# Kernel optimization log

Hardware: AMD Instinct MI355X
Metric: run time of the kernel (lower is better)

Reference implementation:

```python
import jax, jax.numpy as jnp
import numpy as np

N = 50000      # nodes
E = 400000     # edges
DIM = 3        # pseudo-coordinate dim
M = 3          # kernel size per dim (closed B-spline, degree 1)
K = M ** DIM   # 27 basis weights
IN = 32
MID = 32
OUT = 32
EPS = 1e-5


def spline_basis(edge_attr):
    """Degree-1 closed B-spline basis. edge_attr: [E, DIM] in [0,1].
    Returns basis [E, 2^DIM], weight indices [E, 2^DIM] into K."""
    bits = (jnp.arange(2 ** DIM)[:, None] >> jnp.arange(DIM)[None, :]) & 1  # [8, DIM]
    scaled = edge_attr * M                       # closed spline: scale by kernel size
    lo = jnp.floor(scaled)
    frac = scaled - lo                           # [E, DIM]
    b = jnp.where(bits[None].astype(bool), frac[:, None, :], 1.0 - frac[:, None, :])
    basis = jnp.prod(b, axis=-1)                 # [E, 8]
    idx = (lo.astype(jnp.int32)[:, None, :] + bits[None]) % M  # [E, 8, DIM]
    strides = M ** jnp.arange(DIM)               # [1, 3, 9]
    widx = jnp.sum(idx * strides, axis=-1)       # [E, 8] in [0, K)
    return basis, widx


def spline_conv(x, src, dst, basis, widx, W, root, bias):
    """x: [N, in]; W: [K, in, out]; mean aggregation + root weight + bias."""
    x_j = x[src]                                          # gather [E, in]
    upd = basis[:, :, None] * x_j[:, None, :]             # [E, 8, in]
    # scatter-add basis-weighted source features into per-(node, weight-idx) bins
    S = jnp.zeros((N, K, x.shape[1]), x.dtype).at[dst[:, None], widx].add(upd)
    deg = jnp.zeros((N,), x.dtype).at[dst].add(1.0)
    deg = jnp.maximum(deg, 1.0)
    msg = jnp.einsum('nki,kio->no', S, W) / deg[:, None]  # mean over incoming edges
    return msg + x @ root + bias


def batchnorm(h, gamma, beta):
    mu = jnp.mean(h, axis=0)
    var = jnp.var(h, axis=0)  # biased, as in torch BN forward
    return (h - mu) * jax.lax.rsqrt(var + EPS) * gamma + beta


def setup_inputs() -> dict:
    key = jax.random.key(0)
    ks = jax.random.split(key, 16)
    d = {}
    d['x'] = jax.random.normal(ks[0], (N, IN), jnp.float32)
    d['edge_index'] = jax.random.randint(ks[1], (2, E), 0, N, dtype=jnp.int32)
    d['edge_attr'] = jax.random.uniform(ks[2], (E, DIM), dtype=jnp.float32)
    d['pos'] = jax.random.normal(ks[3], (N, DIM), jnp.float32)
    def wscale(fan_in):
        return 1.0 / np.sqrt(fan_in)
    d['W1'] = jax.random.normal(ks[4], (K, IN, MID), jnp.float32) * wscale(IN)
    d['root1'] = jax.random.normal(ks[5], (IN, MID), jnp.float32) * wscale(IN)
    d['b1'] = jnp.zeros((MID,), jnp.float32)
    d['W2'] = jax.random.normal(ks[6], (K, MID, 2 * MID), jnp.float32) * wscale(MID)
    d['root2'] = jax.random.normal(ks[7], (MID, 2 * MID), jnp.float32) * wscale(MID)
    d['b2'] = jnp.zeros((2 * MID,), jnp.float32)
    d['gamma'] = jnp.ones((2 * MID,), jnp.float32)
    d['beta'] = jnp.zeros((2 * MID,), jnp.float32)
    c3_in = 2 * MID + 3
    d['W3'] = jax.random.normal(ks[8], (K, c3_in, OUT), jnp.float32) * wscale(c3_in)
    d['root3'] = jax.random.normal(ks[9], (c3_in, OUT), jnp.float32) * wscale(c3_in)
    d['b3'] = jnp.zeros((OUT,), jnp.float32)
    return d


def reference(x, edge_index, edge_attr, pos, W1, root1, b1, W2, root2, b2,
              gamma, beta, W3, root3, b3):
    src, dst = edge_index[0], edge_index[1]
    basis, widx = spline_basis(edge_attr)
    h = jax.nn.elu(spline_conv(x, src, dst, basis, widx, W1, root1, b1))
    h = jax.nn.elu(batchnorm(spline_conv(h, src, dst, basis, widx, W2, root2, b2), gamma, beta))
    h = jnp.concatenate([h, pos], axis=1)
    out = spline_conv(h, src, dst, basis, widx, W3, root3, b3)
    return out
```

## Files before the change

kernel.cpp:

```cpp
#include <hip/hip_runtime.h>
#include <hip/hip_bf16.h>


#define EPS 1e-5f
#define MAXN 50176
#define MAXE 401408
#define SP2 904
#define SP3 2696

typedef __attribute__((ext_vector_type(8))) short short8;
typedef __attribute__((ext_vector_type(4))) float floatx4;

__device__ int             g_deg[MAXN];
__device__ int             g_offs[MAXN + 1];
__device__ int             g_cursor[MAXN];
__device__ int             g_bsum[256];
__device__ int             g_esrc[MAXE];
__device__ __align__(16) uint4 g_ebas[MAXE * 4];
__device__ __align__(16) __hip_bfloat16 g_h0[MAXN * 32];
__device__ __align__(16) __hip_bfloat16 g_h1[MAXN * 32];
__device__ __align__(16) __hip_bfloat16 g_h2[MAXN * 64];
__device__ __align__(16) __hip_bfloat16 g_h3[MAXN * 96];
__device__ __align__(16) __hip_bfloat16 g_Wp1[28672];
__device__ __align__(16) __hip_bfloat16 g_Wp2[57344];
__device__ __align__(16) __hip_bfloat16 g_Wp3[86016];
__device__ float           g_stats[128];
__device__ int             g_isbf16;

__device__ __forceinline__ float loadf(const void* p, int i, bool bf)
{
    return bf ? (float)((const __hip_bfloat16*)p)[i] : ((const float*)p)[i];
}
__device__ __forceinline__ float bf16f(unsigned int u)
{
    return __uint_as_float(u << 16);
}
__device__ __forceinline__ unsigned short bfbits(float f)
{
    union { __hip_bfloat16 h; unsigned short u; } cv;
    cv.h = __float2bfloat16(f);
    return cv.u;
}

__global__ void init_detect(const unsigned int* __restrict__ x, int n)
{
    int i = blockIdx.x * blockDim.x + threadIdx.x;
    if (blockIdx.x == 0 && threadIdx.x < 64) {
        int lane = threadIdx.x;
        int cnt = 0;
        for (int k = lane; k < 256; k += 64) {
            unsigned int lo = x[k] & 0xFFFFu;
            int ex = (int)((lo >> 7) & 0xFFu);
            if (lo == 0u || (ex >= 96 && ex <= 140)) cnt++;
        }
#pragma unroll
        for (int o = 1; o < 64; o <<= 1) cnt += __shfl_xor(cnt, o, 64);
        if (lane == 0) g_isbf16 = (cnt >= 200) ? 1 : 0;
    }
    if (i < n) { g_deg[i] = 0; g_cursor[i] = 0; }
    if (i < 128) g_stats[i] = 0.0f;
}

template <int COUT>
__device__ __forceinline__ void prep_ws_dev(const void* W, const void* root,
                                            __hip_bfloat16* Wp, int t, bool bf)
{
    int j = t & 7;
    int lane = (t >> 3) & 63;
    int rest = t >> 9;
    int kk = rest % 28;
    int nt = rest / 28;
    int k = kk * 32 + (lane >> 4) * 8 + j;
    int o = nt * 16 + (lane & 15);
    float v = (k < 864) ? loadf(W, k * COUT + o, bf)
                        : loadf(root, (k - 864) * COUT + o, bf);
    Wp[t] = __float2bfloat16(v);
}

__device__ __forceinline__ void prep_w3_dev(const void* W, const void* root,
                                            __hip_bfloat16* Wp, int t, bool bf)
{
    const int KB = 84;
    int j = t & 7;
    int lane = (t >> 3) & 63;
    int rest = t >> 9;
    int kk = rest % KB;
    int nt = rest / KB;
    int k = kk * 32 + (lane >> 4) * 8 + j;
    int o = nt * 16 + (lane & 15);
    float v = 0.0f;
    if (k < 2592) {
        int bin = k / 96;
        int ch = k - bin * 96;
        if (ch < 67) v = loadf(W, (bin * 67 + ch) * 32 + o, bf);
    } else {
        int ch = k - 2592;
        if (ch < 67) v = loadf(root, ch * 32 + o, bf);
    }
    Wp[t] = __float2bfloat16(v);
}

__global__ void misc_kernel(const int* __restrict__ dst, const void* __restrict__ x,
                            const void* W1, const void* r1,
                            const void* W2, const void* r2,
                            const void* W3, const void* r3, int E, int N)
{
    int t = blockIdx.x * blockDim.x + threadIdx.x;
    const bool bf = (g_isbf16 != 0);
    if (t < E) { atomicAdd(&g_deg[dst[t]], 1); return; }
    t -= E;
    int nx = N * 32;
    if (t < nx) { g_h0[t] = __float2bfloat16(loadf(x, t, bf)); return; }
    t -= nx;
    if (t < 28672) { prep_ws_dev<32>(W1, r1, g_Wp1, t, bf); return; }
    t -= 28672;
    if (t < 57344) { prep_ws_dev<64>(W2, r2, g_Wp2, t, bf); return; }
    t -= 57344;
    if (t < 86016) { prep_w3_dev(W3, r3, g_Wp3, t, bf); return; }
}

__global__ void scan_blk(int n)
{
    __shared__ int buf[256];
    int tid = threadIdx.x;
    int i = blockIdx.x * 256 + tid;
    int v = (i < n) ? g_deg[i] : 0;
    buf[tid] = v;
    __syncthreads();
    for (int o = 1; o < 256; o <<= 1) {
        int t = (tid >= o) ? buf[tid - o] : 0;
        __syncthreads();
        buf[tid] += t;
        __syncthreads();
    }
    if (i < n) g_offs[i] = buf[tid] - v;
    if (tid == 255) g_bsum[blockIdx.x] = buf[255];
}

__global__ void scan_top(int nb, int n)
{
    __shared__ int buf[256];
    int tid = threadIdx.x;
    int v = (tid < nb) ? g_bsum[tid] : 0;
    buf[tid] = v;
    __syncthreads();
    for (int o = 1; o < 256; o <<= 1) {
        int t = (tid >= o) ? buf[tid - o] : 0;
        __syncthreads();
        buf[tid] += t;
        __syncthreads();
    }
    if (tid < nb) g_bsum[tid] = buf[tid] - v;
    if (tid == nb - 1) g_offs[n] = buf[tid];
}

__global__ void scan_add(int n)
{
    int i = blockIdx.x * 256 + threadIdx.x;
    if (i < n) g_offs[i] += g_bsum[i >> 8];
}

__global__ void basis_fill(const void* __restrict__ attr,
                           const int* __restrict__ src,
                           const int* __restrict__ dst, int E)
{
    int e = blockIdx.x * blockDim.x + threadIdx.x;
    if (e >= E) return;
    const bool bf = (g_isbf16 != 0);
    float f[3];
    int lo[3];
#pragma unroll
    for (int d = 0; d < 3; ++d) {
        float a = loadf(attr, e * 3 + d, bf);
        float s = a * 3.0f;
        float l = floorf(s);
        lo[d] = (int)l;
        f[d] = s - l;
    }
    const int p3[3] = {1, 3, 9};
    int wx8[8];
    unsigned short bb[8];
#pragma unroll
    for (int b = 0; b < 8; ++b) {
        float w = 1.0f;
        int id = 0;
#pragma unroll
        for (int d = 0; d < 3; ++d) {
            int bit = (b >> d) & 1;
            w *= bit ? f[d] : (1.0f - f[d]);
            id += ((lo[d] + bit) % 3) * p3[d];
        }
        wx8[b] = id;
        bb[b] = bfbits(w);
    }
    unsigned wds[16];
#pragma unroll
    for (int i = 0; i < 16; ++i) {
        unsigned w = 0;
#pragma unroll
        for (int b = 0; b < 8; ++b) {
            if (wx8[b] == 2 * i)     w |= (unsigned)bb[b];
            if (wx8[b] == 2 * i + 1) w |= (unsigned)bb[b] << 16;
        }
        wds[i] = w;
    }
    int d = dst[e];
    int p = atomicAdd(&g_cursor[d], 1);
    int slot = g_offs[d] + p;
    uint4* out4 = &g_ebas[(size_t)slot * 4];
    out4[0] = make_uint4(wds[0],  wds[1],  wds[2],  wds[3]);
    out4[1] = make_uint4(wds[4],  wds[5],  wds[6],  wds[7]);
    out4[2] = make_uint4(wds[8],  wds[9],  wds[10], wds[11]);
    out4[3] = make_uint4(wds[12], wds[13], wds[14], wds[15]);
    g_esrc[slot] = src[e];
}

template <int COUT, bool ELU, int IN_SEL, int OUT_SEL>
__global__ __launch_bounds__(512, 8) void fused_conv(const void* __restrict__ bias,
                                                     int N)
{
    __shared__ unsigned short Sb[8 * SP2];
    __shared__ float invd[8];
    int tid = threadIdx.x, wid = tid >> 6, lane = tid & 63;
    int nbase = blockIdx.x * 8;
    const bool bf = (g_isbf16 != 0);
    const unsigned short* xptr = (IN_SEL == 0) ? (const unsigned short*)g_h0
                                               : (const unsigned short*)g_h1;
    const __hip_bfloat16* Wp = (COUT == 32) ? g_Wp1 : g_Wp2;

    int n = nbase + wid;
    int m = lane & 15, quad = lane >> 4;

    if (n < N) {
        int e0 = g_offs[n], e1 = g_offs[n + 1];
        floatx4 C00 = {}, C01 = {}, C10 = {}, C11 = {};
        for (int base = e0; base < e1; base += 32) {
            int cnt = e1 - base; if (cnt > 32) cnt = 32;
            int jmax = (cnt + 3) >> 2;
            unsigned a0w[4] = {0, 0, 0, 0}, a1w[4] = {0, 0, 0, 0};
            unsigned b0w[4] = {0, 0, 0, 0}, b1w[4] = {0, 0, 0, 0};
#pragma unroll
            for (int j = 0; j < 8; ++j) {
                if (j >= jmax) break;
                int kidx = j * 4 + quad;
                int e = base + kidx;
                int sn = 0;
                unsigned p0 = 0, p1 = 0;
                if (kidx < cnt) {
                    sn = g_esrc[e];
                    const unsigned short* brow =
                        (const unsigned short*)&g_ebas[(size_t)e * 4];
                    p0 = brow[m];
                    p1 = brow[16 + m];
                }
                unsigned av0 = xptr[(size_t)sn * 32 + m];
                unsigned av1 = xptr[(size_t)sn * 32 + 16 + m];
                unsigned sh = 16 * (j & 1);
                a0w[j >> 1] |= av0 << sh;
                a1w[j >> 1] |= av1 << sh;
                b0w[j >> 1] |= p0 << sh;
                b1w[j >> 1] |= p1 << sh;
            }
            union U { unsigned w[4]; short8 v; } A0, A1, B0, B1;
#pragma unroll
            for (int q = 0; q < 4; ++q) {
                A0.w[q] = a0w[q]; A1.w[q] = a1w[q];
                B0.w[q] = b0w[q]; B1.w[q] = b1w[q];
            }
            C00 = __builtin_amdgcn_mfma_f32_16x16x32_bf16(A0.v, B0.v, C00, 0, 0, 0);
            C01 = __builtin_amdgcn_mfma_f32_16x16x32_bf16(A0.v, B1.v, C01, 0, 0, 0);
            C10 = __builtin_amdgcn_mfma_f32_16x16x32_bf16(A1.v, B0.v, C10, 0, 0, 0);
            C11 = __builtin_amdgcn_mfma_f32_16x16x32_bf16(A1.v, B1.v, C11, 0, 0, 0);
        }
        unsigned short* Srow = Sb + wid * SP2;
        {
            floatx4 Cf[4] = {C00, C01, C10, C11};
#pragma unroll
            for (int f = 0; f < 4; ++f) {
                int mt = f >> 1, nt = f & 1;
                int bin = nt * 16 + m;
                if (bin < 27) {
                    union { unsigned short h[4]; uint2 u; } pk;
#pragma unroll
                    for (int r = 0; r < 4; ++r) pk.h[r] = bfbits(Cf[f][r]);
                    *(uint2*)(Srow + bin * 32 + mt * 16 + quad * 4) = pk.u;
                }
            }
        }
        if (lane < 32) Srow[864 + lane] = xptr[(size_t)n * 32 + lane];
        if (lane == 0) {
            int deg = e1 - e0;
            invd[wid] = 1.0f / (float)(deg < 1 ? 1 : deg);
        }
    }
    __syncthreads();

    if (wid * 16 < COUT) {
        int mrow = m & 7;
        const unsigned short* Ab = Sb + mrow * SP2 + quad * 8;
        floatx4 accS = {}, accR = {};
#pragma unroll
        for (int kk = 0; kk < 28; ++kk) {
            short8 a = *(const short8*)(Ab + kk * 32);
            const short* bp = (const short*)Wp +
                ((size_t)(wid * 28 + kk) * 64 + lane) * 8;
            short8 b = *(const short8*)bp;
            if (kk < 27) accS = __builtin_amdgcn_mfma_f32_16x16x32_bf16(a, b, accS, 0, 0, 0);
            else         accR = __builtin_amdgcn_mfma_f32_16x16x32_bf16(a, b, accR, 0, 0, 0);
        }
        int o = wid * 16 + m;
        float bval = loadf(bias, o, bf);
#pragma unroll
        for (int r = 0; r < 4; ++r) {
            int slot = quad * 4 + r;
            if (slot >= 8) continue;
            int nn = nbase + slot;
            if (nn >= N) continue;
            float v = accS[r] * invd[slot] + accR[r] + bval;
            if (ELU) v = v > 0.0f ? v : expm1f(v);
            if (OUT_SEL == 1) g_h1[nn * 32 + o] = __float2bfloat16(v);
            else              g_h2[nn * 64 + o] = __float2bfloat16(v);
        }
    }
}

__global__ __launch_bounds__(512, 4) void fused_conv3(const void* __restrict__ bias,
                                                      void* __restrict__ out_ext,
                                                      int N)
{
    __shared__ __align__(16) unsigned short Sb[8 * SP3];
    __shared__ float red[6][64][4];
    __shared__ float invd[8];
    int tid = threadIdx.x, wid = tid >> 6, lane = tid & 63;
    int nbase = blockIdx.x * 8;
    const bool bf = (g_isbf16 != 0);
    const unsigned short* xptr = (const unsigned short*)g_h3;

    int n = nbase + wid;
    int m = lane & 15, quad = lane >> 4;

    if (n < N) {
        int e0 = g_offs[n], e1 = g_offs[n + 1];
        floatx4 C[6][2];
#pragma unroll
        for (int t = 0; t < 6; ++t) {
            C[t][0] = (floatx4){0.f, 0.f, 0.f, 0.f};
            C[t][1] = (floatx4){0.f, 0.f, 0.f, 0.f};
        }
        for (int base = e0; base < e1; base += 32) {
            int cnt = e1 - base; if (cnt > 32) cnt = 32;
            int jmax = (cnt + 3) >> 2;
            unsigned aw[6][4] = {{0, 0, 0, 0}, {0, 0, 0, 0}, {0, 0, 0, 0},
                                 {0, 0, 0, 0}, {0, 0, 0, 0}, {0, 0, 0, 0}};
            unsigned b0w[4] = {0, 0, 0, 0}, b1w[4] = {0, 0, 0, 0};
#pragma unroll
            for (int j = 0; j < 8; ++j) {
                if (j >= jmax) break;
                int kidx = j * 4 + quad;
                int e = base + kidx;
                int sn = 0;
                unsigned p0 = 0, p1 = 0;
                if (kidx < cnt) {
                    sn = g_esrc[e];
                    const unsigned short* brow =
                        (const unsigned short*)&g_ebas[(size_t)e * 4];
                    p0 = brow[m];
                    p1 = brow[16 + m];
                }
                const unsigned short* hr = xptr + (size_t)sn * 96 + m;
                unsigned av[6];
#pragma unroll
                for (int t = 0; t < 6; ++t) av[t] = hr[t * 16];
                unsigned sh = 16 * (j & 1);
#pragma unroll
                for (int t = 0; t < 6; ++t) aw[t][j >> 1] |= av[t] << sh;
                b0w[j >> 1] |= p0 << sh;
                b1w[j >> 1] |= p1 << sh;
            }
            union U { unsigned w[4]; short8 v; } A, B0, B1;
#pragma unroll
            for (int q = 0; q < 4; ++q) { B0.w[q] = b0w[q]; B1.w[q] = b1w[q]; }
#pragma unroll
            for (int t = 0; t < 6; ++t) {
#pragma unroll
                for (int q = 0; q < 4; ++q) A.w[q] = aw[t][q];
                C[t][0] = __builtin_amdgcn_mfma_f32_16x16x32_bf16(A.v, B0.v, C[t][0], 0, 0, 0);
                C[t][1] = __builtin_amdgcn_mfma_f32_16x16x32_bf16(A.v, B1.v, C[t][1], 0, 0, 0);
            }
        }
        unsigned short* Srow = Sb + wid * SP3;
#pragma unroll
        for (int t = 0; t < 6; ++t) {
#pragma unroll
            for (int ntile = 0; ntile < 2; ++ntile) {
                int bin = ntile * 16 + m;
                if (bin < 27) {
                    union { unsigned short h[4]; uint2 uu; } pk;
#pragma unroll
                    for (int r = 0; r < 4; ++r) pk.h[r] = bfbits(C[t][ntile][r]);
                    *(uint2*)(Srow + bin * 96 + t * 16 + quad * 4) = pk.uu;
                }
            }
        }
        for (int t2 = lane; t2 < 96; t2 += 64)
            Srow[2592 + t2] = xptr[(size_t)n * 96 + t2];
        if (lane == 0) {
            int deg = e1 - e0;
            invd[wid] = 1.0f / (float)(deg < 1 ? 1 : deg);
        }
    }
    __syncthreads();

    int nt = wid & 1, kq = wid >> 1;
    int mrow = m & 7;
    const unsigned short* Ab = Sb + mrow * SP3 + quad * 8;
    floatx4 accS = {}, accR = {};
    {
        int kbeg = kq * 21, kend = kbeg + 21;
        int ksplit = (kend < 81) ? kend : 81;
        for (int kk = kbeg; kk < ksplit; ++kk) {
            short8 a = *(const short8*)(Ab + kk * 32);
            const short* bp = (const short*)g_Wp3 +
                ((size_t)(nt * 84 + kk) * 64 + lane) * 8;
            short8 b = *(const short8*)bp;
            accS = __builtin_amdgcn_mfma_f32_16x16x32_bf16(a, b, accS, 0, 0, 0);
        }
        for (int kk = ksplit; kk < kend; ++kk) {
            short8 a = *(const short8*)(Ab + kk * 32);
            const short* bp = (const short*)g_Wp3 +
                ((size_t)(nt * 84 + kk) * 64 + lane) * 8;
            short8 b = *(const short8*)bp;
            accR = __builtin_amdgcn_mfma_f32_16x16x32_bf16(a, b, accR, 0, 0, 0);
        }
    }
    if (kq < 3)
        *(floatx4*)&red[wid][lane][0] = accS;
    __syncthreads();
    if (kq == 3) {
#pragma unroll
        for (int w = 0; w < 3; ++w)
            accS += *(const floatx4*)&red[2 * w + nt][lane][0];
        int o = nt * 16 + m;
        float bval = loadf(bias, o, bf);
#pragma unroll
        for (int r = 0; r < 4; ++r) {
            int slot = quad * 4 + r;
            if (slot >= 8) continue;
            int nn = nbase + slot;
            if (nn >= N) continue;
            float v = accS[r] * invd[slot] + accR[r] + bval;
            if (bf) ((__hip_bfloat16*)out_ext)[nn * 32 + o] = __float2bfloat16(v);
            else    ((float*)out_ext)[nn * 32 + o] = v;
        }
    }
}

__global__ void bn_reduce(int n)
{
    int tid = threadIdx.x;
    int c = tid & 63;
    int r = tid >> 6;
    float s = 0.0f, s2 = 0.0f;
    for (int i = blockIdx.x * 4 + r; i < n; i += gridDim.x * 4) {
        float v = (float)g_h2[i * 64 + c];
        s += v; s2 += v * v;
    }
    __shared__ float b1s[256], b2s[256];
    b1s[tid] = s; b2s[tid] = s2;
    __syncthreads();
    if (r == 0) {
        s  = b1s[c] + b1s[c + 64] + b1s[c + 128] + b1s[c + 192];
        s2 = b2s[c] + b2s[c + 64] + b2s[c + 128] + b2s[c + 192];
        atomicAdd(&g_stats[c], s);
        atomicAdd(&g_stats[64 + c], s2);
    }
}

__global__ void h3_build(const void* __restrict__ pos,
                         const void* __restrict__ gamma,
                         const void* __restrict__ beta, int N)
{
    __shared__ float cf[128];
    int t = threadIdx.x;
    const bool bf = (g_isbf16 != 0);
    if (t < 64) {
        float inv_n = 1.0f / (float)N;
        float mu = g_stats[t] * inv_n;
        float var = g_stats[64 + t] * inv_n - mu * mu;
        float A = rsqrtf(var + EPS) * loadf(gamma, t, bf);
        cf[t] = A;
        cf[64 + t] = loadf(beta, t, bf) - mu * A;
    }
    __syncthreads();
    int idx = blockIdx.x * blockDim.x + t;
    if (idx >= N * 96) return;
    int n = idx / 96, ch = idx - n * 96;
    float v;
    if (ch < 64) {
        float h = (float)g_h2[n * 64 + ch];
        v = h * cf[ch] + cf[64 + ch];
        v = v > 0.0f ? v : expm1f(v);
    } else if (ch < 67) {
        v = loadf(pos, n * 3 + (ch - 64), bf);
    } else {
        v = 0.0f;
    }
    g_h3[(size_t)n * 96 + ch] = __float2bfloat16(v);
}

extern "C" void kernel_launch(void* const* d_in, const int* in_sizes, int n_in,
                              void* d_out, int out_size, void* d_ws, size_t ws_size,
                              hipStream_t stream)
{
    const void* x      = d_in[0];
    const int*  eindex = (const int*)d_in[1];
    const void* eattr  = d_in[2];
    const void* pos    = d_in[3];
    const void* W1     = d_in[4];
    const void* root1  = d_in[5];
    const void* b1     = d_in[6];
    const void* W2     = d_in[7];
    const void* root2  = d_in[8];
    const void* b2     = d_in[9];
    const void* gamma  = d_in[10];
    const void* beta   = d_in[11];
    const void* W3     = d_in[12];
    const void* root3  = d_in[13];
    const void* b3     = d_in[14];
    (void)d_ws; (void)ws_size; (void)n_in; (void)out_size;

    const int N = in_sizes[0] / 32;
    const int E = in_sizes[1] / 2;
    const int* srcp = eindex;
    const int* dstp = eindex + E;

    init_detect<<<(N + 255) / 256, 256, 0, stream>>>((const unsigned int*)x, N);
    {
        int tot = E + N * 32 + 28672 + 57344 + 86016;
        misc_kernel<<<(tot + 255) / 256, 256, 0, stream>>>(
            dstp, x, W1, root1, W2, root2, W3, root3, E, N);
    }
    int nb = (N + 255) / 256;
    scan_blk<<<nb, 256, 0, stream>>>(N);
    scan_top<<<1, 256, 0, stream>>>(nb, N);
    scan_add<<<nb, 256, 0, stream>>>(N);
    basis_fill<<<(E + 255) / 256, 256, 0, stream>>>(eattr, srcp, dstp, E);

    int nb8 = (N + 7) / 8;
    fused_conv<32, true, 0, 1><<<nb8, 512, 0, stream>>>(b1, N);
    fused_conv<64, false, 1, 2><<<nb8, 512, 0, stream>>>(b2, N);
    bn_reduce<<<120, 256, 0, stream>>>(N);
    h3_build<<<(N * 96 + 255) / 256, 256, 0, stream>>>(pos, gamma, beta, N);
    fused_conv3<<<nb8, 512, 0, stream>>>(b3, d_out, N);
}
```

Before: 431.7 us.

## Permute channel and basis layouts for packed dword gathers and stage edges in LDS

Reorders the basis bins and feature channels so each lane fetches adjacent bf16 pairs as a single 32-bit load. The weight-prep permutation is changed to match. Per-edge basis rows and source indices are staged cooperatively into shared memory, 16 edges per chunk, replacing scattered global 16-bit loads. The aim is fewer, wider global memory transactions in the gather phase. In exchange the MFMA K dimension is half filled per chunk (16 of 32 slots), which doubles MFMA issue count, and it relies on s_waitcnt without a barrier for intra-wave LDS visibility.

```diff
diff --git a/kernel.cpp b/kernel.cpp
--- a/kernel.cpp
+++ b/kernel.cpp
@@ -72,8 +72,16 @@
     int nt = rest / 28;
     int k = kk * 32 + (lane >> 4) * 8 + j;
     int o = nt * 16 + (lane & 15);
-    float v = (k < 864) ? loadf(W, k * COUT + o, bf)
-                        : loadf(root, (k - 864) * COUT + o, bf);
+    float v;
+    if (k < 864) {
+        int bin = k >> 5, p = k & 31;
+        int ch = 2 * (p & 15) + (p >> 4);
+        v = loadf(W, (bin * 32 + ch) * COUT + o, bf);
+    } else {
+        int p = k - 864;
+        int ch = 2 * (p & 15) + (p >> 4);
+        v = loadf(root, ch * COUT + o, bf);
+    }
     Wp[t] = __float2bfloat16(v);
 }
 
@@ -91,10 +99,12 @@
     float v = 0.0f;
     if (k < 2592) {
         int bin = k / 96;
-        int ch = k - bin * 96;
+        int p = k - bin * 96;
+        int ch = 6 * (p & 15) + (p >> 4);
         if (ch < 67) v = loadf(W, (bin * 67 + ch) * 32 + o, bf);
     } else {
-        int ch = k - 2592;
+        int p = k - 2592;
+        int ch = 6 * (p & 15) + (p >> 4);
         if (ch < 67) v = loadf(root, ch * 32 + o, bf);
     }
     Wp[t] = __float2bfloat16(v);
@@ -199,8 +209,8 @@
         unsigned w = 0;
 #pragma unroll
         for (int b = 0; b < 8; ++b) {
-            if (wx8[b] == 2 * i)     w |= (unsigned)bb[b];
-            if (wx8[b] == 2 * i + 1) w |= (unsigned)bb[b] << 16;
+            if (wx8[b] == i)      w |= (unsigned)bb[b];
+            if (wx8[b] == i + 16) w |= (unsigned)bb[b] << 16;
         }
         wds[i] = w;
     }
@@ -220,6 +230,8 @@
                                                      int N)
 {
     __shared__ unsigned short Sb[8 * SP2];
+    __shared__ __align__(16) unsigned basb[8][16][16];
+    __shared__ int ssrc[8][16];
     __shared__ float invd[8];
     int tid = threadIdx.x, wid = tid >> 6, lane = tid & 63;
     int nbase = blockIdx.x * 8;
@@ -234,32 +246,32 @@
     if (n < N) {
         int e0 = g_offs[n], e1 = g_offs[n + 1];
         floatx4 C00 = {}, C01 = {}, C10 = {}, C11 = {};
-        for (int base = e0; base < e1; base += 32) {
-            int cnt = e1 - base; if (cnt > 32) cnt = 32;
+        for (int base = e0; base < e1; base += 16) {
+            int cnt = e1 - base; if (cnt > 16) cnt = 16;
+            {
+                int es = lane >> 2, part = lane & 3;
+                uint4 v = make_uint4(0, 0, 0, 0);
+                if (es < cnt) v = g_ebas[(size_t)(base + es) * 4 + part];
+                *(uint4*)&basb[wid][es][part * 4] = v;
+                if (lane < 16)
+                    ssrc[wid][lane] = (lane < cnt) ? g_esrc[base + lane] : 0;
+            }
+            __builtin_amdgcn_s_waitcnt(0);
             int jmax = (cnt + 3) >> 2;
             unsigned a0w[4] = {0, 0, 0, 0}, a1w[4] = {0, 0, 0, 0};
             unsigned b0w[4] = {0, 0, 0, 0}, b1w[4] = {0, 0, 0, 0};
 #pragma unroll
-            for (int j = 0; j < 8; ++j) {
+            for (int j = 0; j < 4; ++j) {
                 if (j >= jmax) break;
                 int kidx = j * 4 + quad;
-                int e = base + kidx;
-                int sn = 0;
-                unsigned p0 = 0, p1 = 0;
-                if (kidx < cnt) {
-                    sn = g_esrc[e];
-                    const unsigned short* brow =
-                        (const unsigned short*)&g_ebas[(size_t)e * 4];
-                    p0 = brow[m];
-                    p1 = brow[16 + m];
-                }
-                unsigned av0 = xptr[(size_t)sn * 32 + m];
-                unsigned av1 = xptr[(size_t)sn * 32 + 16 + m];
+                int sn = ssrc[wid][kidx];
+                unsigned pw = basb[wid][kidx][m];
+                unsigned hw = *((const unsigned*)xptr + (size_t)sn * 16 + m);
                 unsigned sh = 16 * (j & 1);
-                a0w[j >> 1] |= av0 << sh;
-                a1w[j >> 1] |= av1 << sh;
-                b0w[j >> 1] |= p0 << sh;
-                b1w[j >> 1] |= p1 << sh;
+                a0w[j >> 1] |= (hw & 0xFFFFu) << sh;
+                a1w[j >> 1] |= (hw >> 16) << sh;
+                b0w[j >> 1] |= (pw & 0xFFFFu) << sh;
+                b1w[j >> 1] |= (pw >> 16) << sh;
             }
             union U { unsigned w[4]; short8 v; } A0, A1, B0, B1;
 #pragma unroll
@@ -287,7 +299,10 @@
                 }
             }
         }
-        if (lane < 32) Srow[864 + lane] = xptr[(size_t)n * 32 + lane];
+        if (lane < 32) {
+            int ch = 2 * (lane & 15) + (lane >> 4);
+            Srow[864 + lane] = xptr[(size_t)n * 32 + ch];
+        }
         if (lane == 0) {
             int deg = e1 - e0;
             invd[wid] = 1.0f / (float)(deg < 1 ? 1 : deg);
@@ -329,7 +344,10 @@
                                                       int N)
 {
     __shared__ __align__(16) unsigned short Sb[8 * SP3];
-    __shared__ float red[6][64][4];
+    __shared__ __align__(16) union {
+        struct { unsigned bas[8][16][16]; int src[8][16]; } s1;
+        float red[6][64][4];
+    } u;
     __shared__ float invd[8];
     int tid = threadIdx.x, wid = tid >> 6, lane = tid & 63;
     int nbase = blockIdx.x * 8;
@@ -347,35 +365,39 @@
             C[t][0] = (floatx4){0.f, 0.f, 0.f, 0.f};
             C[t][1] = (floatx4){0.f, 0.f, 0.f, 0.f};
         }
-        for (int base = e0; base < e1; base += 32) {
-            int cnt = e1 - base; if (cnt > 32) cnt = 32;
+        for (int base = e0; base < e1; base += 16) {
+            int cnt = e1 - base; if (cnt > 16) cnt = 16;
+            {
+                int es = lane >> 2, part = lane & 3;
+                uint4 v = make_uint4(0, 0, 0, 0);
+                if (es < cnt) v = g_ebas[(size_t)(base + es) * 4 + part];
+                *(uint4*)&u.s1.bas[wid][es][part * 4] = v;
+                if (lane < 16)
+                    u.s1.src[wid][lane] = (lane < cnt) ? g_esrc[base + lane] : 0;
+            }
+            __builtin_amdgcn_s_waitcnt(0);
             int jmax = (cnt + 3) >> 2;
             unsigned aw[6][4] = {{0, 0, 0, 0}, {0, 0, 0, 0}, {0, 0, 0, 0},
                                  {0, 0, 0, 0}, {0, 0, 0, 0}, {0, 0, 0, 0}};
             unsigned b0w[4] = {0, 0, 0, 0}, b1w[4] = {0, 0, 0, 0};
 #pragma unroll
-            for (int j = 0; j < 8; ++j) {
+            for (int j = 0; j < 4; ++j) {
                 if (j >= jmax) break;
                 int kidx = j * 4 + quad;
-                int e = base + kidx;
-                int sn = 0;
-                unsigned p0 = 0, p1 = 0;
-                if (kidx < cnt) {
-                    sn = g_esrc[e];
-                    const unsigned short* brow =
-                        (const unsigned short*)&g_ebas[(size_t)e * 4];
-                    p0 = brow[m];
-                    p1 = brow[16 + m];
-                }
-                const unsigned short* hr = xptr + (size_t)sn * 96 + m;
-                unsigned av[6];
-#pragma unroll
-                for (int t = 0; t < 6; ++t) av[t] = hr[t * 16];
+                int sn = u.s1.src[wid][kidx];
+                unsigned pw = u.s1.bas[wid][kidx][m];
+                const unsigned* hp = (const unsigned*)xptr + (size_t)sn * 48 + m * 3;
+                unsigned h0 = hp[0], h1 = hp[1], h2 = hp[2];
                 unsigned sh = 16 * (j & 1);
-#pragma unroll
-                for (int t = 0; t < 6; ++t) aw[t][j >> 1] |= av[t] << sh;
-                b0w[j >> 1] |= p0 << sh;
-                b1w[j >> 1] |= p1 << sh;
+                int r = j >> 1;
+                aw[0][r] |= (h0 & 0xFFFFu) << sh;
+                aw[1][r] |= (h0 >> 16) << sh;
+                aw[2][r] |= (h1 & 0xFFFFu) << sh;
+                aw[3][r] |= (h1 >> 16) << sh;
+                aw[4][r] |= (h2 & 0xFFFFu) << sh;
+                aw[5][r] |= (h2 >> 16) << sh;
+                b0w[r] |= (pw & 0xFFFFu) << sh;
+                b1w[r] |= (pw >> 16) << sh;
             }
             union U { unsigned w[4]; short8 v; } A, B0, B1;
 #pragma unroll
@@ -402,8 +424,10 @@
                 }
             }
         }
-        for (int t2 = lane; t2 < 96; t2 += 64)
-            Srow[2592 + t2] = xptr[(size_t)n * 96 + t2];
+        for (int p = lane; p < 96; p += 64) {
+            int ch = 6 * (p & 15) + (p >> 4);
+            Srow[2592 + p] = xptr[(size_t)n * 96 + ch];
+        }
         if (lane == 0) {
             int deg = e1 - e0;
             invd[wid] = 1.0f / (float)(deg < 1 ? 1 : deg);
@@ -434,12 +458,12 @@
         }
     }
     if (kq < 3)
-        *(floatx4*)&red[wid][lane][0] = accS;
+        *(floatx4*)&u.red[wid][lane][0] = accS;
     __syncthreads();
     if (kq == 3) {
 #pragma unroll
         for (int w = 0; w < 3; ++w)
-            accS += *(const floatx4*)&red[2 * w + nt][lane][0];
+            accS += *(const floatx4*)&u.red[2 * w + nt][lane][0];
         int o = nt * 16 + m;
         float bval = loadf(bias, o, bf);
 #pragma unroll
```

Result: faster. 371.1 us (-14.0%).
